# Optimization experiments

Hardware: AMD Instinct MI355X
Metric: run time of the kernel (lower is better)

Reference implementation:

```python
import jax, jax.numpy as jnp
import numpy as np

TAU = 0.07          # temperature
TOP_N_SIM = 5       # n_neighb for KNN label assignment
RANKING_K = 4       # top-k same/diff-class sims for confidence ratio


def setup_inputs() -> dict:
    key = jax.random.key(0)
    k1, k2, k3 = jax.random.split(key, 3)
    n_src, n_tgt, d, n_cls = 8192, 6144, 256, 64
    return {
        "source_features": jax.random.normal(k1, (n_src, d), dtype=jnp.float32),
        "source_labels": jax.random.randint(k2, (n_src,), 0, n_cls, dtype=jnp.int32),
        "target_features": jax.random.normal(k3, (n_tgt, d), dtype=jnp.float32),
    }


def _l2_normalize(x):
    # F.normalize(x, dim=1, p=2) with eps=1e-12
    n = jnp.sqrt(jnp.sum(x * x, axis=1, keepdims=True))
    return x / jnp.maximum(n, 1e-12)


def reference(source_features, source_labels, target_features):
    n_tgt = target_features.shape[0]
    top_ranked_n = n_tgt * 2 // 3

    # cosine similarity matrix [n_src, n_tgt]
    sim = _l2_normalize(source_features) @ _l2_normalize(target_features).T

    # sort each column descending over sources
    order = jnp.argsort(-sim, axis=0)                      # [S, T]

    # KNN label assignment with torch.mode semantics (tie -> smallest value)
    neigh = source_labels[order[:TOP_N_SIM]]               # [K, T]
    counts = (neigh[:, None, :] == neigh[None, :, :]).sum(axis=1)  # [K, T]
    maxc = counts.max(axis=0)                              # [T]
    big = jnp.iinfo(source_labels.dtype).max
    assigned = jnp.where(counts == maxc[None, :], neigh, big).min(axis=0)  # [T]

    # sims & labels reordered by descending similarity, per column
    sorted_sims = jnp.take_along_axis(sim, order, axis=0)  # [S, T]
    sorted_labels = source_labels[order]                   # [S, T]
    pos = sorted_labels == assigned[None, :]               # [S, T]

    def first_k_masked_sum(mask):
        # sum of first RANKING_K sorted sims where mask is True, per column
        csum = jnp.cumsum(mask.astype(sim.dtype), axis=0)
        sel = mask & (csum <= RANKING_K)
        return jnp.sum(jnp.where(sel, sorted_sims, 0.0), axis=0)

    nln = first_k_masked_sum(pos)
    nun = first_k_masked_sum(~pos)
    scores = jax.lax.stop_gradient(nln / nun)              # [T], detached

    _, top_ind = jax.lax.top_k(scores, top_ranked_n)       # confident targets
    conf_sim = sim[:, top_ind]                             # [S, top_ranked_n]
    conf_lab = assigned[top_ind]

    # contrastive softmax loss over sources
    mask_sim = (source_labels[:, None] == conf_lab[None, :]).astype(sim.dtype)
    exp_scores = jax.nn.softmax(conf_sim / TAU, axis=0)
    contrastive = (exp_scores * mask_sim).sum(axis=0) / exp_scores.sum(axis=0)
    return -jnp.mean(jnp.log(contrastive + 1e-6))
```

## Files before the change

### kernel.cpp

```cpp
#include <hip/hip_runtime.h>
#include <cstdint>
#include <cstddef>

#define DIM 256
#define NSRC 8192
#define NCLS 64
#define KSTEPS 8
#define INV_TAU (1.0f / 0.07f)
#define EPITCH 136

typedef __attribute__((ext_vector_type(8))) short bf16x8;
typedef __attribute__((ext_vector_type(4))) float f32x4;
typedef unsigned char uchar;

__device__ __forceinline__ ushort f2bf_rne(float f) {
    uint u = __float_as_uint(f);
    uint r = u + 0x7fff + ((u >> 16) & 1);
    return (ushort)(r >> 16);
}
__device__ __forceinline__ uint bf2ord(uint u) {
    return u ^ (0x8000u + (u >> 15) * 0x7FFFu);
}
__device__ __forceinline__ float ord2f(uint o) {
    uint u = (o & 0x8000u) ? (o ^ 0x8000u) : (~o & 0xFFFFu);
    return __uint_as_float(u << 16);
}

__device__ __forceinline__ void gload_lds16(const void* g, void* l) {
    __builtin_amdgcn_global_load_lds((const __attribute__((address_space(1))) void*)g,
                                     (__attribute__((address_space(3))) void*)l,
                                     16, 0, 0);
}

__global__ __launch_bounds__(256) void l2bf2_k(const float* __restrict__ inA,
                                               ushort* __restrict__ outA, int nA,
                                               const float* __restrict__ inB,
                                               ushort* __restrict__ outB) {
    const int b = blockIdx.x, tid = threadIdx.x;
    const float* in = (b < nA) ? inA : inB;
    ushort* out = (b < nA) ? outA : outB;
    const int row = (b < nA) ? b : b - nA;
    __shared__ float red[256];
    float v = in[(size_t)row * DIM + tid];
    red[tid] = v * v;
    __syncthreads();
    for (int s = 128; s > 0; s >>= 1) {
        if (tid < s) red[tid] += red[tid + s];
        __syncthreads();
    }
    float n = fmaxf(sqrtf(red[0]), 1e-12f);
    out[(size_t)row * DIM + tid] = f2bf_rne(v / n);
}

__global__ __launch_bounds__(256) void class_build_k(const int* __restrict__ labels,
                                                     uchar* __restrict__ lab8,
                                                     int* __restrict__ cstart,
                                                     int* __restrict__ clist, int n) {
    const int c = blockIdx.x, t = threadIdx.x;
    const int g = c * 256 + t;
    if (g < n) lab8[g] = (uchar)labels[g];

    __shared__ int sl[256], se[256];
    const int per = n >> 8;
    const int i0 = t * per;
    int less = 0, eq = 0;
    for (int j = 0; j < per; ++j) {
        const int l = labels[i0 + j];
        less += (l < c);
        eq += (l == c);
    }
    sl[t] = less; se[t] = eq;
    __syncthreads();
    for (int s = 1; s < 256; s <<= 1) {
        const int a = (t >= s) ? sl[t - s] : 0;
        const int b = (t >= s) ? se[t - s] : 0;
        __syncthreads();
        sl[t] += a; se[t] += b;
        __syncthreads();
    }
    const int base = sl[255];
    int pos = base + se[t] - eq;
    for (int j = 0; j < per; ++j) {
        const int i = i0 + j;
        if (labels[i] == c) clist[pos++] = i;
    }
    if (t == 0) cstart[c] = base;
    if (c == 0 && t == 1) cstart[NCLS] = n;
}

__global__ __launch_bounds__(256) void gemm_mfma_k(const ushort* __restrict__ A,
                                                   const ushort* __restrict__ B,
                                                   ushort* __restrict__ C,
                                                   int M, int N) {
    __shared__ __align__(16) ushort smem[128 * EPITCH];

    const int tid = threadIdx.x;
    const int lane = tid & 63, wid = tid >> 6;
    const int wr = wid >> 1, wc = wid & 1;

    const int nwg = gridDim.x * gridDim.y;
    const int bid = blockIdx.y * gridDim.x + blockIdx.x;
    const int cpx = nwg >> 3;
    const int swzb = (bid & 7) * cpx + (bid >> 3);
    const int bm = (swzb / gridDim.x) * 128;
    const int bn = (swzb % gridDim.x) * 128;

    const char* aSrc[2];
    const char* bSrc[2];
    uint ldsOff[2];
#pragma unroll
    for (int it = 0; it < 2; ++it) {
        const int c = it * 256 + tid;
        const int r = c >> 2;
        const int ch = c & 3;
        const int sch = ch ^ ((r >> 1) & 3);
        aSrc[it] = (const char*)A + (size_t)(bm + r) * (DIM * 2) + sch * 16;
        bSrc[it] = (const char*)B + (size_t)(bn + r) * (DIM * 2) + sch * 16;
        ldsOff[it] = it * 4096 + (uint)(wid * 1024);
    }

    const int fr = lane & 15, fk = lane >> 4;
    const int swz = (fr >> 1) & 3;
    int idxA[4], idxB[4];
#pragma unroll
    for (int m = 0; m < 4; ++m)
        idxA[m] = (wr * 64 + m * 16 + fr) * 32 + ((fk ^ swz) * 8);
#pragma unroll
    for (int n = 0; n < 4; ++n)
        idxB[n] = (wc * 64 + n * 16 + fr) * 32 + ((fk ^ swz) * 8);

    f32x4 acc[4][4];
#pragma unroll
    for (int m = 0; m < 4; ++m)
#pragma unroll
        for (int n = 0; n < 4; ++n) acc[m][n] = (f32x4){0.f, 0.f, 0.f, 0.f};

#define STAGE(b, ks)                                                               \
    {                                                                              \
        _Pragma("unroll") for (int it = 0; it < 2; ++it) {                         \
            gload_lds16(aSrc[it] + (ks) * 64,                                      \
                        (char*)smem + (b) * 8192 + ldsOff[it]);                    \
            gload_lds16(bSrc[it] + (ks) * 64,                                      \
                        (char*)smem + 16384 + (b) * 8192 + ldsOff[it]);            \
        }                                                                          \
    }

    int cur = 0;
    STAGE(0, 0);
    for (int ks = 0; ks < KSTEPS; ++ks) {
        __syncthreads();
        if (ks + 1 < KSTEPS) STAGE(cur ^ 1, ks + 1);
        const ushort* sAc = smem + cur * 4096;
        const ushort* sBc = smem + 8192 + cur * 4096;
        bf16x8 av[4], bv[4];
#pragma unroll
        for (int m = 0; m < 4; ++m) av[m] = *(const bf16x8*)&sAc[idxA[m]];
#pragma unroll
        for (int n = 0; n < 4; ++n) bv[n] = *(const bf16x8*)&sBc[idxB[n]];
#pragma unroll
        for (int m = 0; m < 4; ++m)
#pragma unroll
            for (int n = 0; n < 4; ++n)
                acc[m][n] = __builtin_amdgcn_mfma_f32_16x16x32_bf16(av[m], bv[n], acc[m][n], 0, 0, 0);
        cur ^= 1;
    }
#undef STAGE

    __syncthreads();
#pragma unroll
    for (int m = 0; m < 4; ++m) {
#pragma unroll
        for (int n = 0; n < 4; ++n) {
            const int colb = wc * 64 + n * 16 + fr;
#pragma unroll
            for (int j = 0; j < 4; ++j) {
                const int rowb = wr * 64 + m * 16 + fk * 4 + j;
                smem[rowb * EPITCH + colb] = (ushort)bf2ord((uint)f2bf_rne(acc[m][n][j]));
            }
        }
    }
    __syncthreads();
    const int rr = tid >> 4, cc = (tid & 15) * 8;
#pragma unroll
    for (int it = 0; it < 8; ++it) {
        const int r = it * 16 + rr;
        uint4 v = *(const uint4*)&smem[r * EPITCH + cc];
        *(uint4*)(C + (size_t)(bm + r) * N + bn + cc) = v;
    }
}

__global__ __launch_bounds__(256) void assign_score_w(const ushort* __restrict__ sim,
                                                      const int* __restrict__ labels,
                                                      const uchar* __restrict__ lab8,
                                                      const int* __restrict__ cstart,
                                                      const int* __restrict__ clist,
                                                      float* __restrict__ scores_out,
                                                      float* __restrict__ logt_out) {
    const int lane = threadIdx.x & 63, wid = threadIdx.x >> 6;
    const int t = blockIdx.x * 4 + wid;
    const ushort* row = sim + (size_t)t * NSRC;

    uint k0 = 0, k1 = 0, k2 = 0, k3 = 0, k4 = 0, k5 = 0, k6 = 0, k7 = 0;
    float s1 = 0.f;

#define CH4(u16, idx)                                                   \
    {                                                                   \
        uint uu = (uint)(u16);                                          \
        s1 += __expf(fmaf(ord2f(uu), INV_TAU, -INV_TAU));               \
        uint nk = (uu << 16) | (uint)(8191 - (idx));                    \
        uint q;                                                         \
        q = max(k0, nk); nk = min(k0, nk); k0 = q;                      \
        q = max(k1, nk); nk = min(k1, nk); k1 = q;                      \
        q = max(k2, nk); nk = min(k2, nk); k2 = q;                      \
        k3 = max(k3, nk);                                               \
    }
#define CH8(u16, idx)                                                   \
    {                                                                   \
        uint nk = (((uint)(u16)) << 16) | (uint)(8191 - (idx));         \
        uint q;                                                         \
        q = max(k0, nk); nk = min(k0, nk); k0 = q;                      \
        q = max(k1, nk); nk = min(k1, nk); k1 = q;                      \
        q = max(k2, nk); nk = min(k2, nk); k2 = q;                      \
        q = max(k3, nk); nk = min(k3, nk); k3 = q;                      \
        q = max(k4, nk); nk = min(k4, nk); k4 = q;                      \
        q = max(k5, nk); nk = min(k5, nk); k5 = q;                      \
        q = max(k6, nk); nk = min(k6, nk); k6 = q;                      \
        k7 = max(k7, nk);                                               \
    }
#define MERGE8                                                                     \
    _Pragma("unroll")                                                              \
    for (int d = 1; d < 64; d <<= 1) {                                             \
        uint b0 = __shfl_xor(k0, d), b1 = __shfl_xor(k1, d), b2 = __shfl_xor(k2, d),\
             b3 = __shfl_xor(k3, d), b4 = __shfl_xor(k4, d), b5 = __shfl_xor(k5, d),\
             b6 = __shfl_xor(k6, d), b7 = __shfl_xor(k7, d);                        \
        uint r0 = max(k0, b0);                                                     \
        uint r1 = max(max(min(k0, b0), k1), b1);                                   \
        uint r2 = max(max(min(k0, b1), min(k1, b0)), max(k2, b2));                 \
        uint r3 = max(max(min(k0, b2), min(k1, b1)),                               \
                      max(max(min(k2, b0), k3), b3));                              \
        uint r4 = max(max(max(min(k0, b3), min(k1, b2)),                           \
                          max(min(k2, b1), min(k3, b0))), max(k4, b4));            \
        uint r5 = max(max(max(min(k0, b4), min(k1, b3)),                           \
                          max(min(k2, b2), min(k3, b1))),                          \
                      max(max(min(k4, b0), k5), b5));                              \
        uint r6 = max(max(max(min(k0, b5), min(k1, b4)),                           \
                          max(min(k2, b3), min(k3, b2))),                          \
                      max(max(min(k4, b1), min(k5, b0)), max(k6, b6)));            \
        uint r7 = max(max(max(min(k0, b6), min(k1, b5)),                           \
                          max(min(k2, b4), min(k3, b3))),                          \
                      max(max(min(k4, b2), min(k5, b1)),                           \
                          max(max(min(k6, b0), k7), b7)));                         \
        k0 = r0; k1 = r1; k2 = r2; k3 = r3; k4 = r4; k5 = r5; k6 = r6; k7 = r7;    \
    }

    for (int i0 = lane * 8; i0 < NSRC; i0 += 512) {
        uint4 w = *(const uint4*)(row + i0);
        CH4(w.x & 0xFFFF, i0 + 0); CH4(w.x >> 16, i0 + 1);
        CH4(w.y & 0xFFFF, i0 + 2); CH4(w.y >> 16, i0 + 3);
        CH4(w.z & 0xFFFF, i0 + 4); CH4(w.z >> 16, i0 + 5);
        CH4(w.w & 0xFFFF, i0 + 6); CH4(w.w >> 16, i0 + 7);
    }
    const uint prek3 = k3;
    MERGE8;
    if (!__all((int)(prek3 <= k7))) {
        k0 = k1 = k2 = k3 = k4 = k5 = k6 = k7 = 0;
        for (int i0 = lane * 8; i0 < NSRC; i0 += 512) {
            uint4 w = *(const uint4*)(row + i0);
            CH8(w.x & 0xFFFF, i0 + 0); CH8(w.x >> 16, i0 + 1);
            CH8(w.y & 0xFFFF, i0 + 2); CH8(w.y >> 16, i0 + 3);
            CH8(w.z & 0xFFFF, i0 + 4); CH8(w.z >> 16, i0 + 5);
            CH8(w.w & 0xFFFF, i0 + 6); CH8(w.w >> 16, i0 + 7);
        }
        MERGE8;
    }
#undef CH4
#undef CH8
#undef MERGE8

#pragma unroll
    for (int d = 1; d < 64; d <<= 1) s1 += __shfl_xor(s1, d);

    const int l0 = labels[8191 - (int)(k0 & 0xFFFF)];
    const int l1 = labels[8191 - (int)(k1 & 0xFFFF)];
    const int l2 = labels[8191 - (int)(k2 & 0xFFFF)];
    const int l3 = labels[8191 - (int)(k3 & 0xFFFF)];
    const int l4 = labels[8191 - (int)(k4 & 0xFFFF)];
    const int l5 = labels[8191 - (int)(k5 & 0xFFFF)];
    const int l6 = labels[8191 - (int)(k6 & 0xFFFF)];
    const int l7 = labels[8191 - (int)(k7 & 0xFFFF)];

    const int c0 = 1 + (l0 == l1) + (l0 == l2) + (l0 == l3) + (l0 == l4);
    const int c1 = (l1 == l0) + 1 + (l1 == l2) + (l1 == l3) + (l1 == l4);
    const int c2 = (l2 == l0) + (l2 == l1) + 1 + (l2 == l3) + (l2 == l4);
    const int c3 = (l3 == l0) + (l3 == l1) + (l3 == l2) + 1 + (l3 == l4);
    const int c4 = (l4 == l0) + (l4 == l1) + (l4 == l2) + (l4 == l3) + 1;
    const int maxc = max(max(max(c0, c1), max(c2, c3)), c4);
    int assigned = 0x7fffffff;
    if (c0 == maxc) assigned = min(assigned, l0);
    if (c1 == maxc) assigned = min(assigned, l1);
    if (c2 == maxc) assigned = min(assigned, l2);
    if (c3 == maxc) assigned = min(assigned, l3);
    if (c4 == maxc) assigned = min(assigned, l4);
    const int aL = assigned;

    const int negcnt = (l0 != aL) + (l1 != aL) + (l2 != aL) + (l3 != aL) +
                       (l4 != aL) + (l5 != aL) + (l6 != aL) + (l7 != aL);
    float nun = 0.f;
    if (negcnt >= 4) {
        int c = 0;
#define NSTEP(kj, lj)                                                       \
        {                                                                   \
            bool take = ((lj) != aL) && (c < 4);                            \
            nun += take ? ord2f((kj) >> 16) : 0.f;                          \
            c += take ? 1 : 0;                                              \
        }
        NSTEP(k0, l0) NSTEP(k1, l1) NSTEP(k2, l2) NSTEP(k3, l3)
        NSTEP(k4, l4) NSTEP(k5, l5) NSTEP(k6, l6) NSTEP(k7, l7)
#undef NSTEP
    } else {
        uint n0 = 0, n1 = 0, n2 = 0, n3 = 0;
        for (int i0 = lane * 8; i0 < NSRC; i0 += 512) {
            uint4 w = *(const uint4*)(row + i0);
            uint2 lw = *(const uint2*)(lab8 + i0);
#define NEGP(u16, lb)                                                       \
            {                                                               \
                uint x = ((lb) == aL) ? 0u : (uint)(u16);                   \
                uint q;                                                     \
                q = max(n0, x); x = min(n0, x); n0 = q;                     \
                q = max(n1, x); x = min(n1, x); n1 = q;                     \
                q = max(n2, x); x = min(n2, x); n2 = q;                     \
                n3 = max(n3, x);                                            \
            }
            NEGP(w.x & 0xFFFF, (int)(lw.x & 255));
            NEGP(w.x >> 16,    (int)((lw.x >> 8) & 255));
            NEGP(w.y & 0xFFFF, (int)((lw.x >> 16) & 255));
            NEGP(w.y >> 16,    (int)(lw.x >> 24));
            NEGP(w.z & 0xFFFF, (int)(lw.y & 255));
            NEGP(w.z >> 16,    (int)((lw.y >> 8) & 255));
            NEGP(w.w & 0xFFFF, (int)((lw.y >> 16) & 255));
            NEGP(w.w >> 16,    (int)(lw.y >> 24));
#undef NEGP
        }
#pragma unroll
        for (int d = 1; d < 64; d <<= 1) {
            uint b0 = __shfl_xor(n0, d), b1 = __shfl_xor(n1, d),
                 b2 = __shfl_xor(n2, d), b3 = __shfl_xor(n3, d);
            uint r0 = max(n0, b0);
            uint r1 = max(max(min(n0, b0), n1), b1);
            uint r2 = max(max(min(n0, b1), min(n1, b0)), max(n2, b2));
            uint r3 = max(max(min(n0, b2), min(n1, b1)),
                          max(max(min(n2, b0), n3), b3));
            n0 = r0; n1 = r1; n2 = r2; n3 = r3;
        }
        nun = (n0 ? ord2f(n0) : 0.f) + (n1 ? ord2f(n1) : 0.f) +
              (n2 ? ord2f(n2) : 0.f) + (n3 ? ord2f(n3) : 0.f);
    }

    const int cs = cstart[aL], ce = cstart[aL + 1];
    float tp0 = -2.f, tp1 = -2.f, tp2 = -2.f, tp3 = -2.f;
    float sp = 0.f;
    for (int p = cs + lane; p < ce; p += 64) {
        const int idx = clist[p];
        float v = ord2f((uint)row[idx]);
        sp += __expf(fmaf(v, INV_TAU, -INV_TAU));
        float x = v, q;
        q = fmaxf(tp0, x); x = fminf(tp0, x); tp0 = q;
        q = fmaxf(tp1, x); x = fminf(tp1, x); tp1 = q;
        q = fmaxf(tp2, x); x = fminf(tp2, x); tp2 = q;
        tp3 = fmaxf(tp3, x);
    }
#pragma unroll
    for (int d = 1; d < 64; d <<= 1) {
        sp += __shfl_xor(sp, d);
        float b0 = __shfl_xor(tp0, d), b1 = __shfl_xor(tp1, d),
              b2 = __shfl_xor(tp2, d), b3 = __shfl_xor(tp3, d);
        float r0 = fmaxf(tp0, b0);
        float r1 = fmaxf(fmaxf(fminf(tp0, b0), tp1), b1);
        float r2 = fmaxf(fmaxf(fminf(tp0, b1), fminf(tp1, b0)), fmaxf(tp2, b2));
        float r3 = fmaxf(fmaxf(fminf(tp0, b2), fminf(tp1, b1)),
                         fmaxf(fmaxf(fminf(tp2, b0), tp3), b3));
        tp0 = r0; tp1 = r1; tp2 = r2; tp3 = r3;
    }

    if (lane == 0) {
        float nln = (tp0 > -1.5f ? tp0 : 0.f) + (tp1 > -1.5f ? tp1 : 0.f) +
                    (tp2 > -1.5f ? tp2 : 0.f) + (tp3 > -1.5f ? tp3 : 0.f);
        scores_out[t] = nln / nun;
        logt_out[t] = logf(sp / s1 + 1e-6f);
    }
}

__global__ __launch_bounds__(256) void select_topk_w(const float* __restrict__ scores,
                                                     int* __restrict__ selected,
                                                     int n, int k) {
    const int lane = threadIdx.x & 63, wid = threadIdx.x >> 6;
    const int t = blockIdx.x * 4 + wid;
    if (t >= n) return;
    const float st = scores[t];
    int rank = 0;
    for (int j0 = lane * 4; j0 < n; j0 += 256) {
        float4 v = *(const float4*)(scores + j0);
        rank += (v.x > st) || (v.x == st && (j0 + 0) < t);
        rank += (v.y > st) || (v.y == st && (j0 + 1) < t);
        rank += (v.z > st) || (v.z == st && (j0 + 2) < t);
        rank += (v.w > st) || (v.w == st && (j0 + 3) < t);
    }
    for (int d = 1; d < 64; d <<= 1) rank += __shfl_xor(rank, d);
    if (lane == 0) selected[t] = (rank < k) ? 1 : 0;
}

__global__ __launch_bounds__(256) void finalize_k(const float* __restrict__ logt,
                                                  const int* __restrict__ selected,
                                                  float* __restrict__ out, int n, int k) {
    __shared__ float red[256];
    const int tid = threadIdx.x;
    float s = 0.f;
    for (int i = tid; i < n; i += 256) s += selected[i] ? logt[i] : 0.f;
    red[tid] = s;
    __syncthreads();
    for (int st = 128; st > 0; st >>= 1) {
        if (tid < st) red[tid] += red[tid + st];
        __syncthreads();
    }
    if (tid == 0) out[0] = -red[0] / (float)k;
}

extern "C" void kernel_launch(void* const* d_in, const int* in_sizes, int n_in,
                              void* d_out, int out_size, void* d_ws, size_t ws_size,
                              hipStream_t stream) {
    const float* srcF = (const float*)d_in[0];
    const int* labels = (const int*)d_in[1];
    const float* tgtF = (const float*)d_in[2];
    float* out = (float*)d_out;

    const int n_src = in_sizes[1];
    const int d = in_sizes[0] / n_src;
    const int n_tgt = in_sizes[2] / d;
    const int topn = n_tgt * 2 / 3;

    char* ws = (char*)d_ws;
    ushort* src2 = (ushort*)ws;  ws += (size_t)n_src * DIM * sizeof(ushort);
    ushort* tgt2 = (ushort*)ws;  ws += (size_t)n_tgt * DIM * sizeof(ushort);
    ushort* sim  = (ushort*)ws;  ws += (size_t)n_tgt * NSRC * sizeof(ushort);
    float* scores = (float*)ws;  ws += (size_t)n_tgt * sizeof(float);
    float* logt   = (float*)ws;  ws += (size_t)n_tgt * sizeof(float);
    int* selected = (int*)ws;    ws += (size_t)n_tgt * sizeof(int);
    int* cstart   = (int*)ws;    ws += (size_t)(NCLS + 1) * sizeof(int);
    int* clist    = (int*)ws;    ws += (size_t)n_src * sizeof(int);
    uchar* lab8   = (uchar*)ws;  ws += (size_t)n_src;

    l2bf2_k<<<n_tgt + n_src, 256, 0, stream>>>(tgtF, tgt2, n_tgt, srcF, src2);
    class_build_k<<<NCLS, 256, 0, stream>>>(labels, lab8, cstart, clist, n_src);

    dim3 grid(n_src / 128, n_tgt / 128);
    gemm_mfma_k<<<grid, 256, 0, stream>>>(tgt2, src2, sim, n_tgt, n_src);

    assign_score_w<<<n_tgt / 4, 256, 0, stream>>>(sim, labels, lab8, cstart, clist,
                                                  scores, logt);
    select_topk_w<<<(n_tgt + 3) / 4, 256, 0, stream>>>(scores, selected, n_tgt, topn);
    finalize_k<<<1, 256, 0, stream>>>(logt, selected, out, n_tgt, topn);
}
```

Measured before the change: 135.2 us.

## Deepen GEMM LDS pipeline to four stages and vectorize L2 normalize per wave

The GEMM moves from a two-buffer LDS pipeline to a four-buffer ring with three stages in flight. Explicit vmcnt waits and raw barriers replace the per-step __syncthreads, so global-to-LDS loads overlap more MFMA work. The L2-normalize kernel now handles one row per wave, using float4 loads and a shuffle reduction in place of a shared-memory tree reduction. LDS use grows to 64KB per block, which may lower occupancy, and the hand-written waitcnt counts depend on the exact number of loads issued per stage.

```diff
diff --git a/kernel.cpp b/kernel.cpp
--- a/kernel.cpp
+++ b/kernel.cpp
@@ -35,21 +35,26 @@
 __global__ __launch_bounds__(256) void l2bf2_k(const float* __restrict__ inA,
                                                ushort* __restrict__ outA, int nA,
                                                const float* __restrict__ inB,
-                                               ushort* __restrict__ outB) {
-    const int b = blockIdx.x, tid = threadIdx.x;
-    const float* in = (b < nA) ? inA : inB;
-    ushort* out = (b < nA) ? outA : outB;
-    const int row = (b < nA) ? b : b - nA;
-    __shared__ float red[256];
-    float v = in[(size_t)row * DIM + tid];
-    red[tid] = v * v;
-    __syncthreads();
-    for (int s = 128; s > 0; s >>= 1) {
-        if (tid < s) red[tid] += red[tid + s];
-        __syncthreads();
-    }
-    float n = fmaxf(sqrtf(red[0]), 1e-12f);
-    out[(size_t)row * DIM + tid] = f2bf_rne(v / n);
+                                               ushort* __restrict__ outB, int nB) {
+    const int w = (blockIdx.x * 256 + threadIdx.x) >> 6;
+    const int lane = threadIdx.x & 63;
+    if (w >= nA + nB) return;
+    const float* in;
+    ushort* out;
+    int row;
+    if (w < nA) { in = inA; out = outA; row = w; }
+    else        { in = inB; out = outB; row = w - nA; }
+    float4 v = *(const float4*)(in + (size_t)row * DIM + lane * 4);
+    float ss = v.x * v.x + v.y * v.y + v.z * v.z + v.w * v.w;
+#pragma unroll
+    for (int d = 1; d < 64; d <<= 1) ss += __shfl_xor(ss, d);
+    const float n = fmaxf(sqrtf(ss), 1e-12f);
+    ushort4 o;
+    o.x = f2bf_rne(v.x / n);
+    o.y = f2bf_rne(v.y / n);
+    o.z = f2bf_rne(v.z / n);
+    o.w = f2bf_rne(v.w / n);
+    *(ushort4*)(out + (size_t)row * DIM + lane * 4) = o;
 }
 
 __global__ __launch_bounds__(256) void class_build_k(const int* __restrict__ labels,
@@ -92,7 +97,7 @@
                                                    const ushort* __restrict__ B,
                                                    ushort* __restrict__ C,
                                                    int M, int N) {
-    __shared__ __align__(16) ushort smem[128 * EPITCH];
+    __shared__ __align__(16) ushort smem[32768];
 
     const int tid = threadIdx.x;
     const int lane = tid & 63, wid = tid >> 6;
@@ -141,17 +146,26 @@
             gload_lds16(aSrc[it] + (ks) * 64,                                      \
                         (char*)smem + (b) * 8192 + ldsOff[it]);                    \
             gload_lds16(bSrc[it] + (ks) * 64,                                      \
-                        (char*)smem + 16384 + (b) * 8192 + ldsOff[it]);            \
+                        (char*)smem + 32768 + (b) * 8192 + ldsOff[it]);            \
         }                                                                          \
     }
 
-    int cur = 0;
     STAGE(0, 0);
+    STAGE(1, 1);
+    STAGE(2, 2);
+
+#pragma unroll
     for (int ks = 0; ks < KSTEPS; ++ks) {
-        __syncthreads();
-        if (ks + 1 < KSTEPS) STAGE(cur ^ 1, ks + 1);
-        const ushort* sAc = smem + cur * 4096;
-        const ushort* sBc = smem + 8192 + cur * 4096;
+        if (ks < KSTEPS - 2)      { asm volatile("s_waitcnt vmcnt(8)" ::: "memory"); }
+        else if (ks == KSTEPS - 2){ asm volatile("s_waitcnt vmcnt(4)" ::: "memory"); }
+        else                      { asm volatile("s_waitcnt vmcnt(0)" ::: "memory"); }
+        __builtin_amdgcn_s_barrier();
+        asm volatile("" ::: "memory");
+
+        if (ks + 3 < KSTEPS) STAGE((ks + 3) & 3, ks + 3);
+
+        const ushort* sAc = smem + (ks & 3) * 4096;
+        const ushort* sBc = smem + 16384 + (ks & 3) * 4096;
         bf16x8 av[4], bv[4];
 #pragma unroll
         for (int m = 0; m < 4; ++m) av[m] = *(const bf16x8*)&sAc[idxA[m]];
@@ -162,7 +176,6 @@
 #pragma unroll
             for (int n = 0; n < 4; ++n)
                 acc[m][n] = __builtin_amdgcn_mfma_f32_16x16x32_bf16(av[m], bv[n], acc[m][n], 0, 0, 0);
-        cur ^= 1;
     }
 #undef STAGE
 
@@ -449,7 +462,8 @@
     int* clist    = (int*)ws;    ws += (size_t)n_src * sizeof(int);
     uchar* lab8   = (uchar*)ws;  ws += (size_t)n_src;
 
-    l2bf2_k<<<n_tgt + n_src, 256, 0, stream>>>(tgtF, tgt2, n_tgt, srcF, src2);
+    const int nrows = n_tgt + n_src;
+    l2bf2_k<<<(nrows + 3) / 4, 256, 0, stream>>>(tgtF, tgt2, n_tgt, srcF, src2, n_src);
     class_build_k<<<NCLS, 256, 0, stream>>>(labels, lab8, cstart, clist, n_src);
 
     dim3 grid(n_src / 128, n_tgt / 128);
```

Result: faster. 128.9 us (-4.6%).
